# Kernel tuning notes

Hardware: AMD Instinct MI355X
Metric: run time of the kernel (lower is better)

Reference implementation:

```python
import jax, jax.numpy as jnp
import numpy as np

H = 1024
NH = 16
DK = H // NH
FF = 4 * H
EPS = 1e-5

def layer_norm(x, g, b):
    mu = jnp.mean(x, axis=-1, keepdims=True)
    var = jnp.mean(jnp.square(x - mu), axis=-1, keepdims=True)
    return (x - mu) * jax.lax.rsqrt(var + EPS) * g + b

def setup_inputs() -> dict:
    key = jax.random.key(0)
    ks = jax.random.split(key, 12)
    s = 0.02
    return {
        "x": jax.random.normal(ks[0], (2, 2048, H), dtype=jnp.float32),
        "ln_g": jnp.ones((H,), jnp.float32),
        "ln_b": jnp.zeros((H,), jnp.float32),
        "wq": jax.random.normal(ks[1], (H, H), jnp.float32) * s,
        "bq": jnp.zeros((H,), jnp.float32),
        "wk": jax.random.normal(ks[2], (H, H), jnp.float32) * s,
        "bk": jnp.zeros((H,), jnp.float32),
        "wv": jax.random.normal(ks[3], (H, H), jnp.float32) * s,
        "bv": jnp.zeros((H,), jnp.float32),
        "w1": jax.random.normal(ks[4], (H, FF), jnp.float32) * s,
        "b1": jnp.zeros((FF,), jnp.float32),
        "w2": jax.random.normal(ks[5], (FF, H), jnp.float32) * s,
        "b2": jnp.zeros((H,), jnp.float32),
    }

def reference(x, ln_g, ln_b, wq, bq, wk, bk, wv, bv, w1, b1, w2, b2):
    B, S, _ = x.shape
    # Note: the torch module reuses the SAME LayerNorm params for both norms.
    h = layer_norm(x, ln_g, ln_b)
    q = (h @ wq + bq).reshape(B, S, NH, DK).transpose(0, 2, 1, 3)  # [B,NH,S,DK]
    k = (h @ wk + bk).reshape(B, S, NH, DK).transpose(0, 2, 1, 3)
    v = (h @ wv + bv).reshape(B, S, NH, DK).transpose(0, 2, 1, 3)
    scores = jnp.einsum('bhqd,bhkd->bhqk', q, k) / jnp.sqrt(jnp.float32(DK))
    att = jax.nn.softmax(scores, axis=-1)  # [B,NH,S,S]
    att_out = jnp.einsum('bhqk,bhkd->bhqd', att, v)
    att_out = att_out.transpose(0, 2, 1, 3).reshape(B, S, H)
    x = x + att_out  # dropout_prob=0 -> identity
    h2 = layer_norm(x, ln_g, ln_b)
    mlp = jax.nn.gelu(h2 @ w1 + b1, approximate=False) @ w2 + b2
    x = x + mlp
    return (x, att)
```

## Files before the change

kernel.cpp:

```cpp
#include <hip/hip_runtime.h>
#include <hip/hip_bf16.h>

typedef unsigned short u16;
typedef __attribute__((ext_vector_type(8))) short short8;
typedef __attribute__((ext_vector_type(4))) float f32x4;

__device__ inline u16 f2bf(float f) {
    unsigned int u = __float_as_uint(f);
    unsigned int r = (u + 0x7fffu + ((u >> 16) & 1u)) >> 16;
    return (u16)r;
}

__device__ __forceinline__ void gload16(const u16* g, u16* l) {
    __builtin_amdgcn_global_load_lds(
        (const __attribute__((address_space(1))) void*)g,
        (__attribute__((address_space(3))) void*)l, 16, 0, 0);
}

__global__ void transpose_cvt(const float* __restrict__ in, u16* __restrict__ out,
                              int K, int N) {
    __shared__ float tile[32][33];
    int n0 = blockIdx.x * 32, k0 = blockIdx.y * 32;
    int tx = threadIdx.x, ty = threadIdx.y;
#pragma unroll
    for (int i = 0; i < 4; i++)
        tile[ty + i * 8][tx] = in[(size_t)(k0 + ty + i * 8) * N + n0 + tx];
    __syncthreads();
#pragma unroll
    for (int i = 0; i < 4; i++)
        out[(size_t)(n0 + ty + i * 8) * K + k0 + tx] = f2bf(tile[tx][ty + i * 8]);
}

template <bool ADD>
__global__ void ln_kernel(const float* __restrict__ x, const float* __restrict__ add,
                          const float* __restrict__ g, const float* __restrict__ b,
                          float* __restrict__ xa_out, u16* __restrict__ h_out) {
    int row = blockIdx.x;
    int t = threadIdx.x;
    float4 v = ((const float4*)(x + (size_t)row * 1024))[t];
    if (ADD) {
        float4 a = ((const float4*)(add + (size_t)row * 1024))[t];
        v.x += a.x; v.y += a.y; v.z += a.z; v.w += a.w;
        ((float4*)(xa_out + (size_t)row * 1024))[t] = v;
    }
    float s = v.x + v.y + v.z + v.w;
    float sq = v.x * v.x + v.y * v.y + v.z * v.z + v.w * v.w;
#pragma unroll
    for (int off = 32; off >= 1; off >>= 1) {
        s  += __shfl_xor(s, off);
        sq += __shfl_xor(sq, off);
    }
    __shared__ float ps[4], pq[4];
    int wid = t >> 6, lane = t & 63;
    if (lane == 0) { ps[wid] = s; pq[wid] = sq; }
    __syncthreads();
    s  = ps[0] + ps[1] + ps[2] + ps[3];
    sq = pq[0] + pq[1] + pq[2] + pq[3];
    float mu  = s * (1.0f / 1024.0f);
    float var = sq * (1.0f / 1024.0f) - mu * mu;
    float rstd = rsqrtf(var + 1e-5f);
    float4 gv = ((const float4*)g)[t];
    float4 bv = ((const float4*)b)[t];
    ushort4 o;
    o.x = f2bf((v.x - mu) * rstd * gv.x + bv.x);
    o.y = f2bf((v.y - mu) * rstd * gv.y + bv.y);
    o.z = f2bf((v.z - mu) * rstd * gv.z + bv.z);
    o.w = f2bf((v.w - mu) * rstd * gv.w + bv.w);
    ((ushort4*)(h_out + (size_t)row * 1024))[t] = o;
}

template <int BN>
__device__ __forceinline__ void gemm_core(
    const u16* __restrict__ A, const u16* __restrict__ Bt, int K,
    int m0, int n0, u16* As, u16* Bs, f32x4 (*acc)[BN / 32]) {
    const int NB = BN / 32;
    int t = threadIdx.x, lane = t & 63, w = t >> 6;
    int l15 = lane & 15, lhi = lane >> 4;
    int wm = (w >> 1) * 64, wn = (w & 1) * (BN / 2);

    int srow8 = (lane >> 3) & 7;
    int scol = ((lane & 7) ^ srow8) * 8;
    const u16* Ag = A + (size_t)(m0 + w * 32 + (lane >> 3)) * K + scol;
    const u16* Bg = Bt + (size_t)(n0 + w * (BN / 4) + (lane >> 3)) * K + scol;
    u16* AsW = As + (w * 32) * 64;
    u16* BsW = Bs + (w * (BN / 4)) * 64;

    int rs = (l15 & 7) << 3;

    for (int k0 = 0; k0 < K; k0 += 64) {
        __syncthreads();
#pragma unroll
        for (int j = 0; j < 4; j++)
            gload16(Ag + k0 + (size_t)j * 8 * K, AsW + j * 8 * 64);
#pragma unroll
        for (int j = 0; j < NB; j++)
            gload16(Bg + k0 + (size_t)j * 8 * K, BsW + j * 8 * 64);
        __syncthreads();
#pragma unroll
        for (int ks = 0; ks < 2; ks++) {
            short8 af[4], bfr[NB];
#pragma unroll
            for (int mi = 0; mi < 4; mi++)
                af[mi] = *(const short8*)&As[(wm + mi * 16 + l15) * 64 +
                                             ((ks * 32 + lhi * 8) ^ rs)];
#pragma unroll
            for (int ni = 0; ni < NB; ni++)
                bfr[ni] = *(const short8*)&Bs[(wn + ni * 16 + l15) * 64 +
                                              ((ks * 32 + lhi * 8) ^ rs)];
#pragma unroll
            for (int mi = 0; mi < 4; mi++)
#pragma unroll
                for (int ni = 0; ni < NB; ni++)
                    acc[mi][ni] = __builtin_amdgcn_mfma_f32_16x16x32_bf16(
                        af[mi], bfr[ni], acc[mi][ni], 0, 0, 0);
        }
    }
}

__global__ __launch_bounds__(256) void qkv_gemm(
    const u16* __restrict__ A,
    const u16* __restrict__ wqT, const u16* __restrict__ wkT, const u16* __restrict__ wvT,
    const float* __restrict__ bq, const float* __restrict__ bk, const float* __restrict__ bv,
    u16* __restrict__ qb, u16* __restrict__ kb, u16* __restrict__ vtb) {
    __shared__ alignas(16) u16 As[128 * 64];
    __shared__ alignas(16) u16 Bs[128 * 64];
    int z = blockIdx.z;
    const u16* Bt = z == 0 ? wqT : (z == 1 ? wkT : wvT);
    const float* bias = z == 0 ? bq : (z == 1 ? bk : bv);
    float scale = z == 0 ? 0.18033688011112042f : 1.0f;
    int n0 = blockIdx.x * 128, m0 = blockIdx.y * 128;

    f32x4 acc[4][4] = {};
    gemm_core<128>(A, Bt, 1024, m0, n0, As, Bs, acc);

    int t = threadIdx.x, lane = t & 63, w = t >> 6;
    int l15 = lane & 15, lhi = lane >> 4;
    int wm = (w >> 1) * 64, wn = (w & 1) * 64;
#pragma unroll
    for (int mi = 0; mi < 4; mi++)
#pragma unroll
        for (int ni = 0; ni < 4; ni++)
#pragma unroll
            for (int r = 0; r < 4; r++) {
                int row = m0 + wm + mi * 16 + lhi * 4 + r;
                int col = n0 + wn + ni * 16 + l15;
                u16 o = f2bf((acc[mi][ni][r] + bias[col]) * scale);
                int bb = row >> 11, ss = row & 2047, hh = col >> 6, dd = col & 63;
                if (z < 2) {
                    u16* outp = z == 0 ? qb : kb;
                    outp[(((size_t)(bb * 16 + hh) * 2048) + ss) * 64 + dd] = o;
                } else {
                    vtb[(((size_t)(bb * 16 + hh) * 64) + dd) * 2048 + ss] = o;
                }
            }
}

template <int MODE, int BN>
__global__ __launch_bounds__(256) void mlp_gemm(
    const u16* __restrict__ A, const u16* __restrict__ Bt,
    const float* __restrict__ bias, void* __restrict__ outp,
    const float* __restrict__ resid, int N, int K) {
    __shared__ alignas(16) u16 As[128 * 64];
    __shared__ alignas(16) u16 Bs[BN * 64];
    int n0 = blockIdx.x * BN, m0 = blockIdx.y * 128;

    f32x4 acc[4][BN / 32] = {};
    gemm_core<BN>(A, Bt, K, m0, n0, As, Bs, acc);

    int t = threadIdx.x, lane = t & 63, w = t >> 6;
    int l15 = lane & 15, lhi = lane >> 4;
    int wm = (w >> 1) * 64, wn = (w & 1) * (BN / 2);
#pragma unroll
    for (int mi = 0; mi < 4; mi++)
#pragma unroll
        for (int ni = 0; ni < BN / 32; ni++)
#pragma unroll
            for (int r = 0; r < 4; r++) {
                int row = m0 + wm + mi * 16 + lhi * 4 + r;
                int col = n0 + wn + ni * 16 + l15;
                float val = acc[mi][ni][r] + bias[col];
                if (MODE == 2) {
                    float gl = 0.5f * val * (1.0f + erff(val * 0.70710678118654752f));
                    ((u16*)outp)[(size_t)row * N + col] = f2bf(gl);
                } else {
                    ((float*)outp)[(size_t)row * N + col] =
                        val + resid[(size_t)row * N + col];
                }
            }
}

__global__ __launch_bounds__(512) void attn_kernel(
    const u16* __restrict__ q, const u16* __restrict__ k,
    const u16* __restrict__ vt, float* __restrict__ att,
    float* __restrict__ attout) {
    const int S = 2048;
    int bx = blockIdx.x;
    int swz = (bx & 7) * 64 + (bx >> 3);
    int bh = swz >> 4;
    int qb = swz & 15;
    int t = threadIdx.x, w = t >> 6, lane = t & 63;
    int l15 = lane & 15, lhi = lane >> 4;
    int q0 = qb * 128 + w * 16;

    const u16* qh = q + (size_t)bh * S * 64;
    const u16* kh = k + (size_t)bh * S * 64;
    const u16* vh = vt + (size_t)bh * 64 * S;

    __shared__ alignas(16) u16 Ks[2][64][64];
    __shared__ alignas(16) u16 Vs[2][64][64];
    __shared__ alignas(16) float pf_all[8][16 * 36];
    float* pf = pf_all[w];

    int srow = lane >> 3;
    int scol = (((lane & 7) ^ srow)) * 8;
    const u16* kg = kh + (size_t)(w * 8 + srow) * 64 + scol;
    const u16* vg = vh + (size_t)(w * 8 + srow) * 2048 + scol;
    u16* ksl[2] = {&Ks[0][w * 8][0], &Ks[1][w * 8][0]};
    u16* vsl[2] = {&Vs[0][w * 8][0], &Vs[1][w * 8][0]};

    short8 aq0 = *(const short8*)&qh[(size_t)(q0 + l15) * 64 + lhi * 8];
    short8 aq1 = *(const short8*)&qh[(size_t)(q0 + l15) * 64 + 32 + lhi * 8];

    f32x4 z = {0.f, 0.f, 0.f, 0.f};
    float sum[4] = {0.f, 0.f, 0.f, 0.f};

    gload16(kg, ksl[0]);
    for (int i = 0; i < 32; i++) {
        __syncthreads();
        if (i + 1 < 32) gload16(kg + (size_t)(i + 1) * 64 * 64, ksl[(i + 1) & 1]);
        const u16(*Kb)[64] = Ks[i & 1];
#pragma unroll
        for (int sub = 0; sub < 4; sub++) {
            int R = sub * 16 + l15;
            int cs = (R & 7) << 3;
            short8 b0 = *(const short8*)&Kb[R][(lhi * 8) ^ cs];
            short8 b1 = *(const short8*)&Kb[R][(32 + lhi * 8) ^ cs];
            f32x4 s = z;
            s = __builtin_amdgcn_mfma_f32_16x16x32_bf16(aq0, b0, s, 0, 0, 0);
            s = __builtin_amdgcn_mfma_f32_16x16x32_bf16(aq1, b1, s, 0, 0, 0);
#pragma unroll
            for (int r = 0; r < 4; r++) sum[r] += __builtin_exp2f(s[r]);
        }
    }

    float lrl[4];
#pragma unroll
    for (int r = 0; r < 4; r++) {
        float ts = sum[r];
        ts += __shfl_xor(ts, 1);
        ts += __shfl_xor(ts, 2);
        ts += __shfl_xor(ts, 4);
        ts += __shfl_xor(ts, 8);
        lrl[r] = -__log2f(ts);
    }

    f32x4 o[4];
#pragma unroll
    for (int ni = 0; ni < 4; ni++) o[ni] = z;

    float* attq = att + ((size_t)bh * S + q0) * S;
    int sr = lane >> 2, sc = (lane & 3) * 8;

    gload16(kg, ksl[0]);
    gload16(vg, vsl[0]);
    for (int i = 0; i < 32; i++) {
        __syncthreads();
        if (i + 1 < 32) {
            gload16(kg + (size_t)(i + 1) * 64 * 64, ksl[(i + 1) & 1]);
            gload16(vg + (i + 1) * 64, vsl[(i + 1) & 1]);
        }
        const u16(*Kb)[64] = Ks[i & 1];
        const u16(*Vb)[64] = Vs[i & 1];
#pragma unroll
        for (int kp2 = 0; kp2 < 2; kp2++) {
#pragma unroll
            for (int half = 0; half < 2; half++) {
                int R = kp2 * 32 + half * 16 + l15;
                int cs = (R & 7) << 3;
                short8 b0 = *(const short8*)&Kb[R][(lhi * 8) ^ cs];
                short8 b1 = *(const short8*)&Kb[R][(32 + lhi * 8) ^ cs];
                f32x4 s = {lrl[0], lrl[1], lrl[2], lrl[3]};
                s = __builtin_amdgcn_mfma_f32_16x16x32_bf16(aq0, b0, s, 0, 0, 0);
                s = __builtin_amdgcn_mfma_f32_16x16x32_bf16(aq1, b1, s, 0, 0, 0);
#pragma unroll
                for (int r = 0; r < 4; r++)
                    pf[(lhi * 4 + r) * 36 + half * 16 + l15] = __builtin_exp2f(s[r]);
            }
            __builtin_amdgcn_sched_barrier(0);
            asm volatile("s_waitcnt lgkmcnt(0)" ::: "memory");
            __builtin_amdgcn_s_barrier();
            __builtin_amdgcn_sched_barrier(0);
            int ktb = i * 64 + kp2 * 32;
            f32x4 s0 = *(const f32x4*)&pf[sr * 36 + sc];
            f32x4 s1 = *(const f32x4*)&pf[sr * 36 + sc + 4];
            *(f32x4*)&attq[(size_t)sr * S + ktb + sc] = s0;
            *(f32x4*)&attq[(size_t)sr * S + ktb + sc + 4] = s1;
            f32x4 pa0 = *(const f32x4*)&pf[l15 * 36 + lhi * 8];
            f32x4 pa1 = *(const f32x4*)&pf[l15 * 36 + lhi * 8 + 4];
            short8 pa;
            pa[0] = (short)f2bf(pa0[0]); pa[1] = (short)f2bf(pa0[1]);
            pa[2] = (short)f2bf(pa0[2]); pa[3] = (short)f2bf(pa0[3]);
            pa[4] = (short)f2bf(pa1[0]); pa[5] = (short)f2bf(pa1[1]);
            pa[6] = (short)f2bf(pa1[2]); pa[7] = (short)f2bf(pa1[3]);
#pragma unroll
            for (int ni = 0; ni < 4; ni++) {
                int R = ni * 16 + l15;
                int cs = (R & 7) << 3;
                short8 vb = *(const short8*)&Vb[R][(kp2 * 32 + lhi * 8) ^ cs];
                o[ni] = __builtin_amdgcn_mfma_f32_16x16x32_bf16(pa, vb, o[ni], 0, 0, 0);
            }
        }
    }

    int bb = bh >> 4, hh = bh & 15;
#pragma unroll
    for (int ni = 0; ni < 4; ni++)
#pragma unroll
        for (int r = 0; r < 4; r++) {
            int srw = q0 + lhi * 4 + r;
            attout[((size_t)(bb * 2048 + srw)) * 1024 + hh * 64 + ni * 16 + l15] = o[ni][r];
        }
}

extern "C" void kernel_launch(void* const* d_in, const int* in_sizes, int n_in,
                              void* d_out, int out_size, void* d_ws, size_t ws_size,
                              hipStream_t stream) {
    const float* x    = (const float*)d_in[0];
    const float* ln_g = (const float*)d_in[1];
    const float* ln_b = (const float*)d_in[2];
    const float* wq   = (const float*)d_in[3];
    const float* bq   = (const float*)d_in[4];
    const float* wk   = (const float*)d_in[5];
    const float* bk   = (const float*)d_in[6];
    const float* wv   = (const float*)d_in[7];
    const float* bv   = (const float*)d_in[8];
    const float* w1   = (const float*)d_in[9];
    const float* b1   = (const float*)d_in[10];
    const float* w2   = (const float*)d_in[11];
    const float* b2   = (const float*)d_in[12];

    char* ws = (char*)d_ws;
    const size_t MB = 1024 * 1024;
    u16* wqT = (u16*)(ws + 0 * MB);
    u16* wkT = (u16*)(ws + 2 * MB);
    u16* wvT = (u16*)(ws + 4 * MB);
    u16* w1T = (u16*)(ws + 6 * MB);
    u16* w2T = (u16*)(ws + 14 * MB);
    u16* h1  = (u16*)(ws + 22 * MB);
    u16* qb  = (u16*)(ws + 30 * MB);
    u16* kb  = (u16*)(ws + 38 * MB);
    u16* vtb = (u16*)(ws + 46 * MB);
    u16* ub  = (u16*)(ws + 22 * MB);
    float* attout = (float*)(ws + 54 * MB);
    float* xa = (float*)(ws + 70 * MB);
    u16* h2  = (u16*)(ws + 86 * MB);

    float* xout = (float*)d_out;
    float* att  = xout + (size_t)2 * 2048 * 1024;

    dim3 tb(32, 8);
    transpose_cvt<<<dim3(32, 32), tb, 0, stream>>>(wq, wqT, 1024, 1024);
    transpose_cvt<<<dim3(32, 32), tb, 0, stream>>>(wk, wkT, 1024, 1024);
    transpose_cvt<<<dim3(32, 32), tb, 0, stream>>>(wv, wvT, 1024, 1024);
    transpose_cvt<<<dim3(128, 32), tb, 0, stream>>>(w1, w1T, 1024, 4096);
    transpose_cvt<<<dim3(32, 128), tb, 0, stream>>>(w2, w2T, 4096, 1024);

    ln_kernel<false><<<4096, 256, 0, stream>>>(x, nullptr, ln_g, ln_b, nullptr, h1);

    qkv_gemm<<<dim3(8, 32, 3), 256, 0, stream>>>(h1, wqT, wkT, wvT, bq, bk, bv,
                                                 qb, kb, vtb);

    attn_kernel<<<512, 512, 0, stream>>>(qb, kb, vtb, att, attout);

    ln_kernel<true><<<4096, 256, 0, stream>>>(x, attout, ln_g, ln_b, xa, h2);

    mlp_gemm<2, 128><<<dim3(32, 32), 256, 0, stream>>>(h2, w1T, b1, ub, nullptr, 4096, 1024);
    mlp_gemm<3, 64><<<dim3(16, 32), 256, 0, stream>>>(ub, w2T, b2, xout, xa, 1024, 4096);
}
```

Before: 416.4 us.

## Swap MFMA operands for transposed scores and add XCD block swizzle to GEMMs

```diff
diff --git a/kernel.cpp b/kernel.cpp
--- a/kernel.cpp
+++ b/kernel.cpp
@@ -69,6 +69,15 @@
     ((ushort4*)(h_out + (size_t)row * 1024))[t] = o;
 }
 
+__device__ __forceinline__ void xcd_swizzle(int BN, int& m0, int& n0) {
+    int gx = gridDim.x;
+    int lin = blockIdx.x + gx * blockIdx.y;
+    int cpx = (gx * gridDim.y) >> 3;
+    int swz = (lin & 7) * cpx + (lin >> 3);
+    n0 = (swz % gx) * BN;
+    m0 = (swz / gx) * 128;
+}
+
 template <int BN>
 __device__ __forceinline__ void gemm_core(
     const u16* __restrict__ A, const u16* __restrict__ Bt, int K,
@@ -128,7 +137,8 @@
     const u16* Bt = z == 0 ? wqT : (z == 1 ? wkT : wvT);
     const float* bias = z == 0 ? bq : (z == 1 ? bk : bv);
     float scale = z == 0 ? 0.18033688011112042f : 1.0f;
-    int n0 = blockIdx.x * 128, m0 = blockIdx.y * 128;
+    int m0, n0;
+    xcd_swizzle(128, m0, n0);
 
     f32x4 acc[4][4] = {};
     gemm_core<128>(A, Bt, 1024, m0, n0, As, Bs, acc);
@@ -162,7 +172,8 @@
     const float* __restrict__ resid, int N, int K) {
     __shared__ alignas(16) u16 As[128 * 64];
     __shared__ alignas(16) u16 Bs[BN * 64];
-    int n0 = blockIdx.x * BN, m0 = blockIdx.y * 128;
+    int m0, n0;
+    xcd_swizzle(BN, m0, n0);
 
     f32x4 acc[4][BN / 32] = {};
     gemm_core<BN>(A, Bt, K, m0, n0, As, Bs, acc);
@@ -222,7 +233,7 @@
     short8 aq1 = *(const short8*)&qh[(size_t)(q0 + l15) * 64 + 32 + lhi * 8];
 
     f32x4 z = {0.f, 0.f, 0.f, 0.f};
-    float sum[4] = {0.f, 0.f, 0.f, 0.f};
+    float sum = 0.f;
 
     gload16(kg, ksl[0]);
     for (int i = 0; i < 32; i++) {
@@ -236,30 +247,21 @@
             short8 b0 = *(const short8*)&Kb[R][(lhi * 8) ^ cs];
             short8 b1 = *(const short8*)&Kb[R][(32 + lhi * 8) ^ cs];
             f32x4 s = z;
-            s = __builtin_amdgcn_mfma_f32_16x16x32_bf16(aq0, b0, s, 0, 0, 0);
-            s = __builtin_amdgcn_mfma_f32_16x16x32_bf16(aq1, b1, s, 0, 0, 0);
-#pragma unroll
-            for (int r = 0; r < 4; r++) sum[r] += __builtin_exp2f(s[r]);
-        }
-    }
-
-    float lrl[4];
-#pragma unroll
-    for (int r = 0; r < 4; r++) {
-        float ts = sum[r];
-        ts += __shfl_xor(ts, 1);
-        ts += __shfl_xor(ts, 2);
-        ts += __shfl_xor(ts, 4);
-        ts += __shfl_xor(ts, 8);
-        lrl[r] = -__log2f(ts);
-    }
+            s = __builtin_amdgcn_mfma_f32_16x16x32_bf16(b0, aq0, s, 0, 0, 0);
+            s = __builtin_amdgcn_mfma_f32_16x16x32_bf16(b1, aq1, s, 0, 0, 0);
+            sum += __builtin_exp2f(s[0]) + __builtin_exp2f(s[1]) +
+                   __builtin_exp2f(s[2]) + __builtin_exp2f(s[3]);
+        }
+    }
+    sum += __shfl_xor(sum, 16);
+    sum += __shfl_xor(sum, 32);
+    float lrl = -__log2f(sum);
 
     f32x4 o[4];
 #pragma unroll
     for (int ni = 0; ni < 4; ni++) o[ni] = z;
 
     float* attq = att + ((size_t)bh * S + q0) * S;
-    int sr = lane >> 2, sc = (lane & 3) * 8;
 
     gload16(kg, ksl[0]);
     gload16(vg, vsl[0]);
@@ -273,28 +275,26 @@
         const u16(*Vb)[64] = Vs[i & 1];
 #pragma unroll
         for (int kp2 = 0; kp2 < 2; kp2++) {
+            int ktb = i * 64 + kp2 * 32;
 #pragma unroll
             for (int half = 0; half < 2; half++) {
                 int R = kp2 * 32 + half * 16 + l15;
                 int cs = (R & 7) << 3;
                 short8 b0 = *(const short8*)&Kb[R][(lhi * 8) ^ cs];
                 short8 b1 = *(const short8*)&Kb[R][(32 + lhi * 8) ^ cs];
-                f32x4 s = {lrl[0], lrl[1], lrl[2], lrl[3]};
-                s = __builtin_amdgcn_mfma_f32_16x16x32_bf16(aq0, b0, s, 0, 0, 0);
-                s = __builtin_amdgcn_mfma_f32_16x16x32_bf16(aq1, b1, s, 0, 0, 0);
-#pragma unroll
-                for (int r = 0; r < 4; r++)
-                    pf[(lhi * 4 + r) * 36 + half * 16 + l15] = __builtin_exp2f(s[r]);
+                f32x4 s = {lrl, lrl, lrl, lrl};
+                s = __builtin_amdgcn_mfma_f32_16x16x32_bf16(b0, aq0, s, 0, 0, 0);
+                s = __builtin_amdgcn_mfma_f32_16x16x32_bf16(b1, aq1, s, 0, 0, 0);
+                f32x4 p;
+#pragma unroll
+                for (int r = 0; r < 4; r++) p[r] = __builtin_exp2f(s[r]);
+                *(f32x4*)&attq[(size_t)l15 * S + ktb + half * 16 + lhi * 4] = p;
+                *(f32x4*)&pf[l15 * 36 + half * 16 + lhi * 4] = p;
             }
             __builtin_amdgcn_sched_barrier(0);
             asm volatile("s_waitcnt lgkmcnt(0)" ::: "memory");
             __builtin_amdgcn_s_barrier();
             __builtin_amdgcn_sched_barrier(0);
-            int ktb = i * 64 + kp2 * 32;
-            f32x4 s0 = *(const f32x4*)&pf[sr * 36 + sc];
-            f32x4 s1 = *(const f32x4*)&pf[sr * 36 + sc + 4];
-            *(f32x4*)&attq[(size_t)sr * S + ktb + sc] = s0;
-            *(f32x4*)&attq[(size_t)sr * S + ktb + sc + 4] = s1;
             f32x4 pa0 = *(const f32x4*)&pf[l15 * 36 + lhi * 8];
             f32x4 pa1 = *(const f32x4*)&pf[l15 * 36 + lhi * 8 + 4];
             short8 pa;
```

New measurement: 427.5 us. 2.7% more time.
